# Optimization experiments

Hardware: AMD Instinct MI355X
Metric: run time of the kernel (lower is better)

Reference implementation:

```python
import jax, jax.numpy as jnp
import numpy as np

N_INP = 256
N_OUT = 16
H = 1024
UH = 32  # uni_hidden_unit
BATCH = 16384


def setup_inputs() -> dict:
    key = jax.random.key(0)
    ks = jax.random.split(key, 16)
    s = 0.02
    return {
        "x": jax.random.normal(ks[0], (BATCH, N_INP), dtype=jnp.float32),
        # main MLP: n_inp -> 1024 -> 1024 -> n_out
        "W0": jax.random.normal(ks[1], (N_INP, H), dtype=jnp.float32) * s,
        "b0": jnp.zeros((H,), jnp.float32),
        "W1": jax.random.normal(ks[2], (H, H), dtype=jnp.float32) * s,
        "b1": jnp.zeros((H,), jnp.float32),
        "W2": jax.random.normal(ks[3], (H, N_OUT), dtype=jnp.float32) * s,
        "b2": jnp.zeros((N_OUT,), jnp.float32),
        # stacked per-feature uni MLPs: 1 -> UH -> UH -> n_out, one per feature
        "uw1": jax.random.normal(ks[4], (N_INP, UH), dtype=jnp.float32) * s,
        "ub1": jnp.zeros((N_INP, UH), jnp.float32),
        "uw2": jax.random.normal(ks[5], (N_INP, UH, UH), dtype=jnp.float32) * s,
        "ub2": jnp.zeros((N_INP, UH), jnp.float32),
        "uw3": jax.random.normal(ks[6], (N_INP, UH, N_OUT), dtype=jnp.float32) * s,
        "ub3": jnp.zeros((N_INP, N_OUT), jnp.float32),
    }


def reference(x, W0, b0, W1, b1, W2, b2, uw1, ub1, uw2, ub2, uw3, ub3):
    # main MLP: Linear+ReLU, Linear+ReLU, Linear
    y = jax.nn.relu(x @ W0 + b0)
    y = jax.nn.relu(y @ W1 + b1)
    y = y @ W2 + b2  # [B, n_out]

    # per-feature univariate MLPs, vectorized over the feature axis i
    # input to uni MLP i is x[:, i:i+1]  -> first Linear(1, UH)
    h = jax.nn.relu(x[:, :, None] * uw1[None] + ub1[None])       # [B, I, UH]
    h = jax.nn.relu(jnp.einsum('bif,ifo->bio', h, uw2) + ub2[None])  # [B, I, UH]
    u = jnp.einsum('bif,ifo->bio', h, uw3) + ub3[None]           # [B, I, n_out]
    return y + u.sum(axis=1)
```

## Files before the change

### kernel.cpp

```cpp
#include <hip/hip_runtime.h>

typedef unsigned short u16;
typedef __attribute__((ext_vector_type(4))) float f32x4;
typedef __attribute__((ext_vector_type(4))) int i32x4;
typedef __attribute__((ext_vector_type(8))) short short8;
typedef __attribute__((ext_vector_type(8))) __bf16 bf16x8;
typedef __attribute__((ext_vector_type(4))) unsigned short u16x4;

#define BATCH 16384
#define NINP 256
#define HID 1024
#define NOUT 16

__device__ __forceinline__ u16 f2bf(float f) {
  unsigned u = __builtin_bit_cast(unsigned, f);
  u += 0x7FFFu + ((u >> 16) & 1u);
  return (u16)(u >> 16);
}
__device__ __forceinline__ f32x4 mfma_s8(short8 a, short8 b, f32x4 c) {
  return __builtin_amdgcn_mfma_f32_16x16x32_bf16(
      __builtin_bit_cast(bf16x8, a), __builtin_bit_cast(bf16x8, b), c, 0, 0, 0);
}
__device__ __forceinline__ f32x4 mfma_bb(bf16x8 a, bf16x8 b, f32x4 c) {
  return __builtin_amdgcn_mfma_f32_16x16x32_bf16(a, b, c, 0, 0, 0);
}
__device__ __forceinline__ void gload_lds16(const void* g, void* l) {
  __builtin_amdgcn_global_load_lds(
      (const __attribute__((address_space(1))) void*)g,
      (__attribute__((address_space(3))) void*)l, 16, 0, 0);
}

static const size_t OFF_H0   = 0;
static const size_t OFF_PART = 0;
static const size_t OFF_H1   = 33554432;
static const size_t OFF_XB   = 33554432;
static const size_t OFF_W0T  = 67108864;
static const size_t OFF_W1T  = 67633152;
static const size_t OFF_W2T  = 69730304;
static const size_t OFF_UWP  = 69763072;
static const size_t OFF_CB   = 70811648;


__global__ __launch_bounds__(256) void k_prep(
    const float* __restrict__ x,
    const float* __restrict__ W0, const float* __restrict__ W1,
    const float* __restrict__ W2,
    const float* __restrict__ uw1, const float* __restrict__ ub1,
    const float* __restrict__ uw2, const float* __restrict__ ub2,
    const float* __restrict__ uw3, const float* __restrict__ b2,
    const float* __restrict__ ub3,
    u16* __restrict__ xb,
    u16* __restrict__ W0T, u16* __restrict__ W1T, u16* __restrict__ W2T,
    char* __restrict__ uwp, float* __restrict__ cb)
{
  __shared__ float tile[32][33];
  const int bid = blockIdx.x;
  const int tid = threadIdx.x;

  if (bid < 1312) {
    const float* src; u16* dst; int K, N, kb, ob;
    if (bid < 256)       { src = W0; dst = W0T; K = 256;  N = 1024; int t = bid;        kb = (t & 7) * 32;  ob = (t >> 3) * 32; }
    else if (bid < 1280) { src = W1; dst = W1T; K = 1024; N = 1024; int t = bid - 256;  kb = (t & 31) * 32; ob = (t >> 5) * 32; }
    else                 { src = W2; dst = W2T; K = 1024; N = 16;   int t = bid - 1280; kb = t * 32;        ob = 0; }
    const int tx = tid & 31, ty = tid >> 5;
    for (int r = ty; r < 32; r += 8)
      if (ob + tx < N) tile[r][tx] = src[(size_t)(kb + r) * N + ob + tx];
    __syncthreads();
    for (int r = ty; r < 32; r += 8)
      if (ob + r < N) dst[(size_t)(ob + r) * K + kb + tx] = f2bf(tile[tx][r]);
  } else if (bid < 5408) {
    const int idx = ((bid - 1312) * 256 + tid) * 4;
    const float4 v = *(const float4*)&x[idx];
    u16x4 o4 = { f2bf(v.x), f2bf(v.y), f2bf(v.z), f2bf(v.w) };
    *(u16x4*)&xb[idx] = o4;
  } else if (bid < 5664) {
    const int e = ((bid - 5408) * 256 + tid) * 4;
    const float4 v = *(const float4*)&uw2[e];
    const int i = e >> 10, f = (e >> 5) & 31, o = e & 31;
    const float vv[4] = { v.x, v.y, v.z, v.w };
    u16* blob16 = (u16*)(uwp + (size_t)i * 4096);
#pragma unroll
    for (int d = 0; d < 4; ++d) {
      const int oo = o + d;
      const int lane = ((f >> 3) << 4) | (oo & 15);
      blob16[256 + (oo >> 4) * 512 + lane * 8 + (f & 7)] = f2bf(vv[d]);
    }
  } else if (bid < 5792) {
    const int e = ((bid - 5664) * 256 + tid) * 4;
    const float4 v = *(const float4*)&uw3[e];
    const int i = e >> 9, f = (e >> 4) & 31, o2 = e & 15;
    const int s = (f < 16) ? (((f >> 2) << 3) + (f & 3))
                           : ((((f - 16) >> 2) << 3) + 4 + (f & 3));
    const float vv[4] = { v.x, v.y, v.z, v.w };
    u16* blob16 = (u16*)(uwp + (size_t)i * 4096);
#pragma unroll
    for (int d = 0; d < 4; ++d)
      blob16[1280 + ((s >> 3) * 16 + o2 + d) * 8 + (s & 7)] = f2bf(vv[d]);
  } else if (bid < 5816) {
    const int e4 = (bid - 5792) * 256 + tid;
    const int i = e4 / 24, r4 = e4 % 24;
    const float* src = (r4 < 8)  ? &uw1[i * 32 + r4 * 4]
                     : (r4 < 16) ? &ub1[i * 32 + (r4 - 8) * 4]
                                 : &ub2[i * 32 + (r4 - 16) * 4];
    *(float4*)(uwp + (size_t)i * 4096 + r4 * 16) = *(const float4*)src;
  } else {
    __shared__ float red[16][16];
    const int ig = tid >> 4, o = tid & 15;
    float s = 0.f;
#pragma unroll
    for (int k = 0; k < 16; ++k) s += ub3[(ig * 16 + k) * 16 + o];
    red[ig][o] = s;
    __syncthreads();
    if (tid < 16) {
      float t = b2[tid];
#pragma unroll
      for (int k = 0; k < 16; ++k) t += red[k][tid];
      cb[tid] = t;
    }
  }
}

__global__ __launch_bounds__(256, 2) void k_gemm(
    const u16* __restrict__ A, const u16* __restrict__ BT,
    const float* __restrict__ bias, u16* __restrict__ C,
    int M, int N, int K)
{
  const int tid = threadIdx.x;
  const int lane = tid & 63, wid = tid >> 6;
  const int l15 = lane & 15, g = lane >> 4;
  const int nbn = N >> 7;
  const int nwg = gridDim.x;
  int logical = blockIdx.x;
  if ((nwg & 7) == 0) {
    const int q = nwg >> 3;
    logical = (logical & 7) * q + (logical >> 3);
  }
  const int bm = logical / nbn, bn = logical % nbn;
  const size_t rb = (size_t)bm * 128, cbase = (size_t)bn * 128;

  __shared__ __align__(16) u16 As[128 * 32];
  __shared__ __align__(16) u16 Bs[128 * 32];

  const int wr = (wid >> 1) * 64, wc = (wid & 1) * 64;
  f32x4 acc[4][4] = {};

  for (int kt = 0; kt < K; kt += 32) {
#pragma unroll
    for (int it = 0; it < 2; ++it) {
      const int s = it * 256 + tid;
      const int row = s >> 2, kc = s & 3;
      gload_lds16(&A[(rb + row) * K + kt + kc * 8], &As[s * 8]);
      gload_lds16(&BT[(cbase + row) * K + kt + kc * 8], &Bs[s * 8]);
    }
    __syncthreads();
    short8 a[4], b[4];
#pragma unroll
    for (int m = 0; m < 4; ++m)
      a[m] = *(const short8*)&As[(wr + m * 16 + l15) * 32 + g * 8];
#pragma unroll
    for (int n = 0; n < 4; ++n)
      b[n] = *(const short8*)&Bs[(wc + n * 16 + l15) * 32 + g * 8];
#pragma unroll
    for (int m = 0; m < 4; ++m)
#pragma unroll
      for (int n = 0; n < 4; ++n)
        acc[m][n] = mfma_s8(a[m], b[n], acc[m][n]);
    __syncthreads();
  }

#pragma unroll
  for (int n = 0; n < 4; ++n) {
    const int col = (int)cbase + wc + n * 16 + l15;
    const float bv = bias[col];
#pragma unroll
    for (int m = 0; m < 4; ++m) {
#pragma unroll
      for (int r = 0; r < 4; ++r) {
        const int row = (int)rb + wr + m * 16 + g * 4 + r;
        float v = acc[m][n][r] + bv;
        v = fmaxf(v, 0.f);
        C[(size_t)row * N + col] = f2bf(v);
      }
    }
  }
}

__global__ __launch_bounds__(256, 4) void k_uni(
    const float* __restrict__ x,
    const char* __restrict__ uwp,
    const u16* __restrict__ H1, const u16* __restrict__ W2T,
    float* __restrict__ part)
{
  const int tid = threadIdx.x, lane = tid & 63, wid = tid >> 6;
  const int l15 = lane & 15, g = lane >> 4;
  const int chunk = blockIdx.x & 7, rowblk = blockIdx.x >> 3;
  const int rb_blk = rowblk * 128;
  const int rb = rb_blk + wid * 32;
  const int i0 = chunk * 32;

  __shared__ __align__(16) float xt[128][33];
  __shared__ __align__(16) char wbuf[2][4096];

  {
    const int r0 = tid >> 3, c4 = (tid & 7) << 2;
#pragma unroll
    for (int rr = 0; rr < 128; rr += 32)
      *(float4*)&xt[rr + r0][c4] =
          *(const float4*)&x[(size_t)(rb_blk + rr + r0) * NINP + i0 + c4];
  }
  gload_lds16(uwp + (size_t)i0 * 4096 + tid * 16, &wbuf[0][tid * 16]);
  __syncthreads();

  const f32x4 zero4 = {0.f, 0.f, 0.f, 0.f};
  f32x4 acc0 = zero4, acc1 = zero4;
  const float* xr0 = &xt[wid * 32 + l15][0];
  const float* xr1 = &xt[wid * 32 + 16 + l15][0];

#pragma unroll 2
  for (int ii = 0; ii < 32; ++ii) {
    const int nxt = (ii + 1) & 31;
    gload_lds16(uwp + (size_t)(i0 + nxt) * 4096 + tid * 16,
                &wbuf[(ii + 1) & 1][tid * 16]);

    const char* bp = &wbuf[ii & 1][0];
    const f32x4 w1lo = *(const f32x4*)(bp + g * 32);
    const f32x4 w1hi = *(const f32x4*)(bp + g * 32 + 16);
    const f32x4 b1lo = *(const f32x4*)(bp + 128 + g * 32);
    const f32x4 b1hi = *(const f32x4*)(bp + 128 + g * 32 + 16);
    const f32x4 bb0  = *(const f32x4*)(bp + 256 + g * 16);
    const f32x4 bb1  = *(const f32x4*)(bp + 320 + g * 16);
    const bf16x8 bv0 = *(const bf16x8*)(bp + 512 + lane * 16);
    const bf16x8 bv1 = *(const bf16x8*)(bp + 1536 + lane * 16);
    const bf16x8 b3  = *(const bf16x8*)(bp + 2560 + lane * 16);
    const float xv0 = xr0[ii], xv1 = xr1[ii];

    bf16x8 af0, af1;
#pragma unroll
    for (int j = 0; j < 4; ++j) {
      af0[j]     = (__bf16)fmaxf(fmaf(xv0, w1lo[j], b1lo[j]), 0.f);
      af0[4 + j] = (__bf16)fmaxf(fmaf(xv0, w1hi[j], b1hi[j]), 0.f);
      af1[j]     = (__bf16)fmaxf(fmaf(xv1, w1lo[j], b1lo[j]), 0.f);
      af1[4 + j] = (__bf16)fmaxf(fmaf(xv1, w1hi[j], b1hi[j]), 0.f);
    }

    const f32x4 d00 = mfma_bb(bv0, af0, bb0);
    const f32x4 d10 = mfma_bb(bv1, af0, bb1);
    const f32x4 d01 = mfma_bb(bv0, af1, bb0);
    const f32x4 d11 = mfma_bb(bv1, af1, bb1);

    bf16x8 h20, h21;
#pragma unroll
    for (int j = 0; j < 4; ++j) {
      h20[j]     = (__bf16)fmaxf(d00[j], 0.f);
      h20[4 + j] = (__bf16)fmaxf(d10[j], 0.f);
      h21[j]     = (__bf16)fmaxf(d01[j], 0.f);
      h21[4 + j] = (__bf16)fmaxf(d11[j], 0.f);
    }

    acc0 = mfma_bb(b3, h20, acc0);
    acc1 = mfma_bb(b3, h21, acc1);

    __syncthreads();
  }

  {
    const int kb0 = chunk * 128;
#pragma unroll
    for (int kk = 0; kk < 4; ++kk) {
      const int kb = kb0 + kk * 32;
      const bf16x8 a0 = __builtin_bit_cast(bf16x8,
          *(const i32x4*)&H1[(size_t)(rb + l15) * HID + kb + g * 8]);
      const bf16x8 a1 = __builtin_bit_cast(bf16x8,
          *(const i32x4*)&H1[(size_t)(rb + 16 + l15) * HID + kb + g * 8]);
      const bf16x8 bv = __builtin_bit_cast(bf16x8,
          *(const i32x4*)&W2T[l15 * HID + kb + g * 8]);
      acc0 = mfma_bb(bv, a0, acc0);
      acc1 = mfma_bb(bv, a1, acc1);
    }
  }

  float* p = part + ((size_t)chunk * BATCH + rb) * NOUT;
  *(f32x4*)&p[l15 * 16 + g * 4] = acc0;
  *(f32x4*)&p[(16 + l15) * 16 + g * 4] = acc1;
}

__global__ __launch_bounds__(256) void k_reduce(
    const float* __restrict__ part, const float* __restrict__ cb,
    float* __restrict__ out)
{
  const int j4 = blockIdx.x * 256 + threadIdx.x;
  const float4 c = ((const float4*)cb)[j4 & 3];
  const float4* p = (const float4*)part;
  float rx = c.x, ry = c.y, rz = c.z, rw = c.w;
#pragma unroll
  for (int cc = 0; cc < 8; ++cc) {
    const float4 a = p[cc * 65536 + j4];
    rx += a.x; ry += a.y; rz += a.z; rw += a.w;
  }
  float4 r; r.x = rx; r.y = ry; r.z = rz; r.w = rw;
  ((float4*)out)[j4] = r;
}

extern "C" void kernel_launch(void* const* d_in, const int* in_sizes, int n_in,
                              void* d_out, int out_size, void* d_ws, size_t ws_size,
                              hipStream_t stream) {
  (void)in_sizes; (void)n_in; (void)out_size; (void)ws_size;
  const float* x   = (const float*)d_in[0];
  const float* W0  = (const float*)d_in[1];
  const float* b0  = (const float*)d_in[2];
  const float* W1  = (const float*)d_in[3];
  const float* b1  = (const float*)d_in[4];
  const float* W2  = (const float*)d_in[5];
  const float* b2  = (const float*)d_in[6];
  const float* uw1 = (const float*)d_in[7];
  const float* ub1 = (const float*)d_in[8];
  const float* uw2 = (const float*)d_in[9];
  const float* ub2 = (const float*)d_in[10];
  const float* uw3 = (const float*)d_in[11];
  const float* ub3 = (const float*)d_in[12];
  float* out = (float*)d_out;

  char* ws = (char*)d_ws;
  u16*   H0   = (u16*)(ws + OFF_H0);
  u16*   H1   = (u16*)(ws + OFF_H1);
  u16*   xb   = (u16*)(ws + OFF_XB);
  u16*   W0T  = (u16*)(ws + OFF_W0T);
  u16*   W1T  = (u16*)(ws + OFF_W1T);
  u16*   W2T  = (u16*)(ws + OFF_W2T);
  char*  uwp  = (char*)(ws + OFF_UWP);
  float* cb   = (float*)(ws + OFF_CB);
  float* part = (float*)(ws + OFF_PART);

  k_prep<<<5817, 256, 0, stream>>>(x, W0, W1, W2, uw1, ub1, uw2, ub2, uw3,
                                   b2, ub3, xb, W0T, W1T, W2T, uwp, cb);
  k_gemm<<<1024, 256, 0, stream>>>(xb, W0T, b0, H0, BATCH, HID, NINP);
  k_gemm<<<1024, 256, 0, stream>>>(H0, W1T, b1, H1, BATCH, HID, HID);
  k_uni<<<1024, 256, 0, stream>>>(x, uwp, H1, W2T, part);
  k_reduce<<<256, 256, 0, stream>>>(part, cb, out);
}
```

Before: 105.4 us.

## Replace GEMM with 256x256 double-buffered 8-wave kernel using swizzled LDS

The two MLP GEMMs now use a 512-thread, 256x256-tile kernel with 64-wide K steps. It double-buffers A/B tiles in 128 KB of dynamic LDS, using an XOR swizzle to avoid bank conflicts. Global-to-LDS loads for the next tile are interleaved between MFMA phases, with barriers and s_setprio to overlap memory with compute and raise reuse per loaded byte. This costs far more LDS and registers per block and gives only 256 blocks, so occupancy and per-iteration barrier overhead could limit gains.

Result: slower. 109.8 us (+4.2%).

```diff
diff --git a/kernel.cpp b/kernel.cpp
--- a/kernel.cpp
+++ b/kernel.cpp
@@ -3,7 +3,6 @@
 typedef unsigned short u16;
 typedef __attribute__((ext_vector_type(4))) float f32x4;
 typedef __attribute__((ext_vector_type(4))) int i32x4;
-typedef __attribute__((ext_vector_type(8))) short short8;
 typedef __attribute__((ext_vector_type(8))) __bf16 bf16x8;
 typedef __attribute__((ext_vector_type(4))) unsigned short u16x4;
 
@@ -16,10 +15,6 @@
   unsigned u = __builtin_bit_cast(unsigned, f);
   u += 0x7FFFu + ((u >> 16) & 1u);
   return (u16)(u >> 16);
-}
-__device__ __forceinline__ f32x4 mfma_s8(short8 a, short8 b, f32x4 c) {
-  return __builtin_amdgcn_mfma_f32_16x16x32_bf16(
-      __builtin_bit_cast(bf16x8, a), __builtin_bit_cast(bf16x8, b), c, 0, 0, 0);
 }
 __device__ __forceinline__ f32x4 mfma_bb(bf16x8 a, bf16x8 b, f32x4 c) {
   return __builtin_amdgcn_mfma_f32_16x16x32_bf16(a, b, c, 0, 0, 0);
@@ -39,7 +34,6 @@
 static const size_t OFF_W2T  = 69730304;
 static const size_t OFF_UWP  = 69763072;
 static const size_t OFF_CB   = 70811648;
-
 
 __global__ __launch_bounds__(256) void k_prep(
     const float* __restrict__ x,
@@ -120,68 +114,140 @@
   }
 }
 
-__global__ __launch_bounds__(256, 2) void k_gemm(
+__global__ __launch_bounds__(512, 2) void k_gemm8(
     const u16* __restrict__ A, const u16* __restrict__ BT,
     const float* __restrict__ bias, u16* __restrict__ C,
     int M, int N, int K)
 {
+  extern __shared__ __align__(16) char lds[];
   const int tid = threadIdx.x;
   const int lane = tid & 63, wid = tid >> 6;
   const int l15 = lane & 15, g = lane >> 4;
-  const int nbn = N >> 7;
-  const int nwg = gridDim.x;
+  const int wA = wid >> 2;
+  const int wn = wid & 3;
+  const int nbn = N >> 8;
   int logical = blockIdx.x;
-  if ((nwg & 7) == 0) {
-    const int q = nwg >> 3;
-    logical = (logical & 7) * q + (logical >> 3);
-  }
-  const int bm = logical / nbn, bn = logical % nbn;
-  const size_t rb = (size_t)bm * 128, cbase = (size_t)bn * 128;
-
-  __shared__ __align__(16) u16 As[128 * 32];
-  __shared__ __align__(16) u16 Bs[128 * 32];
-
-  const int wr = (wid >> 1) * 64, wc = (wid & 1) * 64;
-  f32x4 acc[4][4] = {};
-
-  for (int kt = 0; kt < K; kt += 32) {
-#pragma unroll
-    for (int it = 0; it < 2; ++it) {
-      const int s = it * 256 + tid;
-      const int row = s >> 2, kc = s & 3;
-      gload_lds16(&A[(rb + row) * K + kt + kc * 8], &As[s * 8]);
-      gload_lds16(&BT[(cbase + row) * K + kt + kc * 8], &Bs[s * 8]);
-    }
-    __syncthreads();
-    short8 a[4], b[4];
+  { const int nwg = gridDim.x;
+    if ((nwg & 7) == 0) { const int q = nwg >> 3; logical = (logical & 7) * q + (logical >> 3); } }
+  const int bm = logical / nbn, bn = logical - bm * nbn;
+  const size_t rb = (size_t)bm * 256, cb = (size_t)bn * 256;
+
+  const int q7 = l15 & 7;
+  const int arow0 = wA * 128 + l15;
+  const int brow0 = wn * 64 + l15;
+
+  char* const ldsA = lds;
+  char* const ldsB = lds + 65536;
+
+  const u16* Ag = A + rb * K;
+  const u16* Bg = BT + cb * K;
+
+  f32x4 acc[8][4] = {};
+  const int NT = K >> 6;
+
+#define STAGE(arr, src, ktE, s) do { \
+    const int G_ = (s) * 512 + tid; \
+    const int row_ = G_ >> 3; \
+    const int c8_ = (G_ & 7) ^ (row_ & 7); \
+    gload_lds16(&(src)[(size_t)row_ * K + (ktE) + c8_ * 8], (arr) + G_ * 16); \
+  } while (0)
+
+#define ARD(bp, m, kk) (*(const bf16x8*)((bp) + (((arow0 + (m) * 16) * 8 + (((kk) * 4 + g) ^ q7)) << 4)))
+#define BRD(bp, n, kk) (*(const bf16x8*)((bp) + (((brow0 + (n) * 16) * 8 + (((kk) * 4 + g) ^ q7)) << 4)))
+
+#pragma unroll
+  for (int s = 0; s < 4; ++s) STAGE(ldsA, Ag, 0, s);
+#pragma unroll
+  for (int s = 0; s < 4; ++s) STAGE(ldsB, Bg, 0, s);
+  asm volatile("s_waitcnt vmcnt(0)" ::: "memory");
+  __builtin_amdgcn_s_barrier();
+
+  for (int t = 0; t < NT; ++t) {
+    const int b = t & 1;
+    const char* Ab = ldsA + b * 32768;
+    const char* Bb = ldsB + b * 32768;
+    char* An = ldsA + (b ^ 1) * 32768;
+    char* Bn = ldsB + (b ^ 1) * 32768;
+    const int kt1 = (t + 1) << 6;
+    const bool stg = (t + 1 < NT);
+    bf16x8 av[4][2], bv0[2][2], bv1[2][2];
+
+#pragma unroll
+    for (int m = 0; m < 4; ++m) { av[m][0] = ARD(Ab, m, 0); av[m][1] = ARD(Ab, m, 1); }
+#pragma unroll
+    for (int n = 0; n < 2; ++n) { bv0[n][0] = BRD(Bb, n, 0); bv0[n][1] = BRD(Bb, n, 1); }
+    if (stg) { STAGE(An, Ag, kt1, 0); STAGE(Bn, Bg, kt1, 0); }
+    __builtin_amdgcn_s_barrier();
+    __builtin_amdgcn_s_setprio(1);
 #pragma unroll
     for (int m = 0; m < 4; ++m)
-      a[m] = *(const short8*)&As[(wr + m * 16 + l15) * 32 + g * 8];
-#pragma unroll
-    for (int n = 0; n < 4; ++n)
-      b[n] = *(const short8*)&Bs[(wc + n * 16 + l15) * 32 + g * 8];
+#pragma unroll
+      for (int n = 0; n < 2; ++n) {
+        acc[m][n] = mfma_bb(av[m][0], bv0[n][0], acc[m][n]);
+        acc[m][n] = mfma_bb(av[m][1], bv0[n][1], acc[m][n]);
+      }
+    __builtin_amdgcn_s_setprio(0);
+    __builtin_amdgcn_s_barrier();
+
+#pragma unroll
+    for (int n = 0; n < 2; ++n) { bv1[n][0] = BRD(Bb, n + 2, 0); bv1[n][1] = BRD(Bb, n + 2, 1); }
+    if (stg) { STAGE(An, Ag, kt1, 1); STAGE(Bn, Bg, kt1, 1); STAGE(An, Ag, kt1, 2); }
+    __builtin_amdgcn_s_barrier();
+    __builtin_amdgcn_s_setprio(1);
 #pragma unroll
     for (int m = 0; m < 4; ++m)
 #pragma unroll
-      for (int n = 0; n < 4; ++n)
-        acc[m][n] = mfma_s8(a[m], b[n], acc[m][n]);
-    __syncthreads();
-  }
-
+      for (int n = 0; n < 2; ++n) {
+        acc[m][n + 2] = mfma_bb(av[m][0], bv1[n][0], acc[m][n + 2]);
+        acc[m][n + 2] = mfma_bb(av[m][1], bv1[n][1], acc[m][n + 2]);
+      }
+    __builtin_amdgcn_s_setprio(0);
+    __builtin_amdgcn_s_barrier();
+
+#pragma unroll
+    for (int m = 0; m < 4; ++m) { av[m][0] = ARD(Ab, m + 4, 0); av[m][1] = ARD(Ab, m + 4, 1); }
+    if (stg) { STAGE(Bn, Bg, kt1, 2); STAGE(An, Ag, kt1, 3); STAGE(Bn, Bg, kt1, 3); }
+    __builtin_amdgcn_s_barrier();
+    __builtin_amdgcn_s_setprio(1);
+#pragma unroll
+    for (int m = 0; m < 4; ++m)
+#pragma unroll
+      for (int n = 0; n < 2; ++n) {
+        acc[m + 4][n + 2] = mfma_bb(av[m][0], bv1[n][0], acc[m + 4][n + 2]);
+        acc[m + 4][n + 2] = mfma_bb(av[m][1], bv1[n][1], acc[m + 4][n + 2]);
+      }
+    __builtin_amdgcn_s_setprio(0);
+    __builtin_amdgcn_s_barrier();
+
+    __builtin_amdgcn_s_setprio(1);
+#pragma unroll
+    for (int m = 0; m < 4; ++m)
+#pragma unroll
+      for (int n = 0; n < 2; ++n) {
+        acc[m + 4][n] = mfma_bb(av[m][0], bv0[n][0], acc[m + 4][n]);
+        acc[m + 4][n] = mfma_bb(av[m][1], bv0[n][1], acc[m + 4][n]);
+      }
+    __builtin_amdgcn_s_setprio(0);
+    asm volatile("s_waitcnt vmcnt(0)" ::: "memory");
+    __builtin_amdgcn_s_barrier();
+  }
+#undef STAGE
+#undef ARD
+#undef BRD
+
+  const int colb = (int)cb + wn * 64;
+  const int rowb = (int)rb + wA * 128;
 #pragma unroll
   for (int n = 0; n < 4; ++n) {
-    const int col = (int)cbase + wc + n * 16 + l15;
-    const float bv = bias[col];
-#pragma unroll
-    for (int m = 0; m < 4; ++m) {
+    const int col = colb + n * 16 + l15;
+    const float bvs = bias[col];
+#pragma unroll
+    for (int m = 0; m < 8; ++m)
 #pragma unroll
       for (int r = 0; r < 4; ++r) {
-        const int row = (int)rb + wr + m * 16 + g * 4 + r;
-        float v = acc[m][n][r] + bv;
-        v = fmaxf(v, 0.f);
-        C[(size_t)row * N + col] = f2bf(v);
+        const int row = rowb + m * 16 + g * 4 + r;
+        C[(size_t)row * N + col] = f2bf(fmaxf(acc[m][n][r] + bvs, 0.f));
       }
-    }
   }
 }
 
@@ -331,10 +397,13 @@
   float* cb   = (float*)(ws + OFF_CB);
   float* part = (float*)(ws + OFF_PART);
 
+  hipFuncSetAttribute((const void*)k_gemm8,
+                      hipFuncAttributeMaxDynamicSharedMemorySize, 131072);
+
   k_prep<<<5817, 256, 0, stream>>>(x, W0, W1, W2, uw1, ub1, uw2, ub2, uw3,
                                    b2, ub3, xb, W0T, W1T, W2T, uwp, cb);
-  k_gemm<<<1024, 256, 0, stream>>>(xb, W0T, b0, H0, BATCH, HID, NINP);
-  k_gemm<<<1024, 256, 0, stream>>>(H0, W1T, b1, H1, BATCH, HID, HID);
+  k_gemm8<<<256, 512, 131072, stream>>>(xb, W0T, b0, H0, BATCH, HID, NINP);
+  k_gemm8<<<256, 512, 131072, stream>>>(H0, W1T, b1, H1, BATCH, HID, HID);
   k_uni<<<1024, 256, 0, stream>>>(x, uwp, H1, W2T, part);
   k_reduce<<<256, 256, 0, stream>>>(part, cb, out);
 }
```
